# Optimization experiments

Hardware: AMD Instinct MI355X
Metric: run time of the kernel (lower is better)

## Reference

```python
import jax, jax.numpy as jnp
import numpy as np

TEMPERATURE = 0.07
B, D = 8192, 512
NUM_CLASSES = 100


def setup_inputs() -> dict:
    key = jax.random.key(0)
    k1, k2 = jax.random.split(key)
    x = jax.random.normal(k1, (B, D), dtype=jnp.float32)
    # docstring: embeddings are normalized over D
    embeds = x / jnp.linalg.norm(x, axis=-1, keepdims=True)
    labels = jax.random.randint(k2, (B,), 0, NUM_CLASSES, dtype=jnp.int64)
    return {"embeds": embeds, "labels": labels}


def reference(embeds, labels):
    n = embeds.shape[0]
    logits = (embeds @ embeds.T) / TEMPERATURE  # (B, B)
    same_label = labels[None, :] == labels[:, None]  # (B, B), symmetric
    neg_inf = jnp.array(-jnp.inf, dtype=logits.dtype)
    # denominator base: logsumexp over different-label entries of each column
    denom_activations = jnp.where(same_label, neg_inf, logits)
    base_denom_row = jax.nn.logsumexp(denom_activations, axis=0)  # (B,)
    # base_denom[i, j] = base_denom_row[i] (torch code repeats along dim 1)
    in_numer = same_label & ~jnp.eye(n, dtype=bool)
    numer_count = in_numer.sum(axis=0)  # (B,) positives per column
    # log_denom = logaddexp(logit, base) on in_numer entries; ce = log_denom - logit
    log_denom = jnp.logaddexp(logits, base_denom_row[:, None])
    ce = jnp.where(in_numer, log_denom - logits, 0.0)
    loss = jnp.sum(ce / numer_count.astype(ce.dtype)) / n
    return loss
```

## Files before the change

### kernel.cpp

```cpp
#include <hip/hip_runtime.h>
#include <hip/hip_bf16.h>
#include <math.h>

#define NB 8192
#define ND 512
#define NCLS 100

constexpr float INV_T = 1.0f / 0.07f;
constexpr float MAXL  = 1.0f / 0.07f;

typedef __attribute__((ext_vector_type(8))) short short8v;
typedef __attribute__((ext_vector_type(4))) float f32x4;

__device__ __forceinline__ ushort f2bf(float x) {
    uint32_t u = __float_as_uint(x);
    uint32_t r = (u + 0x7FFFu + ((u >> 16) & 1u)) >> 16;
    return (ushort)r;
}
__device__ __forceinline__ float bf2f(short v) {
    return __uint_as_float(((uint32_t)(ushort)v) << 16);
}

__global__ __launch_bounds__(256) void setup_kernel(const int* __restrict__ labels,
                                                    int* cls_cnt, int* cls_off,
                                                    int* cls_cur, int* members,
                                                    int* pair_off, double* accum) {
    __shared__ int s_cnt[NCLS];
    const int t = threadIdx.x;
    if (t < NCLS) s_cnt[t] = 0;
    if (t == 0) *accum = 0.0;
    __syncthreads();
    for (int j = t; j < NB; j += blockDim.x) atomicAdd(&s_cnt[labels[j]], 1);
    __syncthreads();
    if (t < NCLS) cls_cnt[t] = s_cnt[t];
    __syncthreads();
    if (t == 0) {
        int off = 0, poff = 0;
        for (int c = 0; c < NCLS; ++c) {
            cls_off[c] = off; cls_cur[c] = off; off += s_cnt[c];
            pair_off[c] = poff; poff += s_cnt[c] * s_cnt[c];
        }
        pair_off[NCLS] = poff;
    }
    __syncthreads();
    for (int j = t; j < NB; j += blockDim.x) {
        const int c = labels[j];
        const int pos = atomicAdd(&cls_cur[c], 1);
        members[pos] = j;
    }
}

__global__ __launch_bounds__(256) void convert_kernel(const float* __restrict__ E,
                                                      ushort* __restrict__ Ebf,
                                                      float* __restrict__ rowsum) {
    const int idx = blockIdx.x * 256 + threadIdx.x;
    const float4 v = ((const float4*)E)[idx];
    ushort4 o;
    o.x = f2bf(v.x); o.y = f2bf(v.y); o.z = f2bf(v.z); o.w = f2bf(v.w);
    ((ushort4*)Ebf)[idx] = o;
    if (idx < NB) rowsum[idx] = 0.f;
}

__global__ __launch_bounds__(256) void pass1_mfma_kernel(const ushort* __restrict__ Ebf,
                                                         const int* __restrict__ labels,
                                                         float* __restrict__ rowsum) {
    __shared__ ushort Atile[128 * 64];
    __shared__ ushort Btile[128 * 64];
    __shared__ float  s_rowsum[128];
    __shared__ int    s_labi[128];
    __shared__ int    s_labj[128];

    const int t    = threadIdx.x;
    const int lane = t & 63;
    const int w    = t >> 6;
    const int wr   = (w >> 1) * 64;
    const int wc   = (w & 1) * 64;
    const int cl   = lane & 15;
    const int rg   = lane >> 4;

    const int j0 = blockIdx.x * 128;
    const int i0 = blockIdx.y * 128;

    if (t < 128) { s_rowsum[t] = 0.f; s_labi[t] = labels[i0 + t]; }
    else         { s_labj[t - 128] = labels[j0 + t - 128]; }

    f32x4 acc[4][4];
    #pragma unroll
    for (int m = 0; m < 4; ++m)
        #pragma unroll
        for (int n = 0; n < 4; ++n)
            acc[m][n] = (f32x4){0.f, 0.f, 0.f, 0.f};

    for (int ks = 0; ks < ND / 64; ++ks) {
        if (ks) __syncthreads();
        {
            const ushort* asrc = Ebf + (size_t)i0 * ND + ks * 64;
            const ushort* bsrc = Ebf + (size_t)j0 * ND + ks * 64;
            #pragma unroll
            for (int q = 0; q < 4; ++q) {
                const int o    = (w * 4 + q) * 1024 + lane * 16;
                const int row  = o >> 7;
                const int slot = (o & 127) >> 4;
                const int sl2  = slot ^ (row & 7);
                __builtin_amdgcn_global_load_lds(
                    (const __attribute__((address_space(1))) unsigned int*)(asrc + row * ND + sl2 * 8),
                    (__attribute__((address_space(3))) unsigned int*)((char*)Atile + (w * 4 + q) * 1024),
                    16, 0, 0);
                __builtin_amdgcn_global_load_lds(
                    (const __attribute__((address_space(1))) unsigned int*)(bsrc + row * ND + sl2 * 8),
                    (__attribute__((address_space(3))) unsigned int*)((char*)Btile + (w * 4 + q) * 1024),
                    16, 0, 0);
            }
        }
        __syncthreads();

        #pragma unroll
        for (int kk = 0; kk < 2; ++kk) {
            short8v a[4], b[4];
            #pragma unroll
            for (int m = 0; m < 4; ++m) {
                const int row = wr + m * 16 + cl;
                const int sl  = (kk * 4 + rg) ^ (row & 7);
                a[m] = *(const short8v*)(Atile + row * 64 + sl * 8);
            }
            #pragma unroll
            for (int n = 0; n < 4; ++n) {
                const int row = wc + n * 16 + cl;
                const int sl  = (kk * 4 + rg) ^ (row & 7);
                b[n] = *(const short8v*)(Btile + row * 64 + sl * 8);
            }
            #pragma unroll
            for (int m = 0; m < 4; ++m)
                #pragma unroll
                for (int n = 0; n < 4; ++n)
                    acc[m][n] = __builtin_amdgcn_mfma_f32_16x16x32_bf16(a[m], b[n], acc[m][n], 0, 0, 0);
        }
    }

    int ljn[4];
    #pragma unroll
    for (int n = 0; n < 4; ++n) ljn[n] = s_labj[wc + n * 16 + cl];

    #pragma unroll
    for (int m = 0; m < 4; ++m) {
        #pragma unroll
        for (int reg = 0; reg < 4; ++reg) {
            const int rloc = wr + m * 16 + rg * 4 + reg;
            const int li   = s_labi[rloc];
            float s = 0.f;
            #pragma unroll
            for (int n = 0; n < 4; ++n) {
                const float d = acc[m][n][reg];
                const float e = __expf(fmaf(d, INV_T, -MAXL));
                s += (ljn[n] != li) ? e : 0.f;
            }
            s += __shfl_xor(s, 1, 64);
            s += __shfl_xor(s, 2, 64);
            s += __shfl_xor(s, 4, 64);
            s += __shfl_xor(s, 8, 64);
            if (cl == 0) atomicAdd(&s_rowsum[rloc], s);
        }
    }
    __syncthreads();
    if (t < 128) atomicAdd(&rowsum[i0 + t], s_rowsum[t]);
}

__global__ __launch_bounds__(256) void pass2_pairs_kernel(const ushort* __restrict__ Ebf,
                                                          const float* __restrict__ rowsum,
                                                          const int* __restrict__ cls_cnt,
                                                          const int* __restrict__ cls_off,
                                                          const int* __restrict__ members,
                                                          const int* __restrict__ pair_off,
                                                          double* __restrict__ accum) {
    __shared__ int    s_off[NCLS + 1];
    __shared__ double sd[4];
    const int t = threadIdx.x;
    for (int k = t; k <= NCLS; k += 256) s_off[k] = pair_off[k];
    __syncthreads();
    const int P = s_off[NCLS];

    const int g  = t >> 3;
    const int s  = t & 7;

    double dlocal = 0.0;
    for (int p = blockIdx.x * 32 + g; p < P; p += gridDim.x * 32) {
        int lo = 0, hi = NCLS - 1;
        while (lo < hi) {
            const int mid = (lo + hi + 1) >> 1;
            if (s_off[mid] <= p) lo = mid; else hi = mid - 1;
        }
        const int c  = lo;
        const int mc = cls_cnt[c];
        const int q  = p - s_off[c];
        const int a  = q / mc;
        const int b  = q - a * mc;
        if (a == b) continue;
        const int i = members[cls_off[c] + a];
        const int j = members[cls_off[c] + b];

        const ushort* ei = Ebf + (size_t)i * ND + s * 8;
        const ushort* ej = Ebf + (size_t)j * ND + s * 8;
        float d = 0.f;
        #pragma unroll
        for (int it = 0; it < 8; ++it) {
            const short8v x = *(const short8v*)(ei + it * 64);
            const short8v y = *(const short8v*)(ej + it * 64);
            #pragma unroll
            for (int e = 0; e < 8; ++e)
                d = fmaf(bf2f(x[e]), bf2f(y[e]), d);
        }
        d += __shfl_xor(d, 1, 64);
        d += __shfl_xor(d, 2, 64);
        d += __shfl_xor(d, 4, 64);
        if (s == 0) {
            const float base = MAXL + logf(rowsum[i]);
            const float xv   = base - d * INV_T;
            const float sp   = fmaxf(xv, 0.f) + log1pf(__expf(-fabsf(xv)));
            dlocal += (double)(sp / (float)(mc - 1));
        }
    }

    #pragma unroll
    for (int o2 = 32; o2 >= 1; o2 >>= 1) dlocal += __shfl_xor(dlocal, o2, 64);
    const int lane = t & 63, w = t >> 6;
    if (lane == 0) sd[w] = dlocal;
    __syncthreads();
    if (t == 0) {
        const double tot = sd[0] + sd[1] + sd[2] + sd[3];
        if (tot != 0.0) atomicAdd(accum, tot);
    }
}

__global__ void finalize_kernel(const double* __restrict__ accum, float* __restrict__ out) {
    if (threadIdx.x == 0 && blockIdx.x == 0)
        out[0] = (float)(accum[0] / (double)NB);
}

#define TI 16
#define TJ 4
#define THREADS 256

__global__ __launch_bounds__(THREADS) void pass1_f32_kernel(const float* __restrict__ E,
                                                            const int* __restrict__ labels,
                                                            float* __restrict__ base_row) {
    __shared__ float e_tile[TI][ND];
    __shared__ int   s_rowlab[TI];
    __shared__ float s_part[4][TI];

    const int t  = threadIdx.x;
    const int i0 = blockIdx.x * TI;

    {
        const float4* src = (const float4*)(E + (size_t)i0 * ND);
        float4* dst = (float4*)(&e_tile[0][0]);
        #pragma unroll
        for (int k = 0; k < (TI * ND / 4) / THREADS; ++k)
            dst[t + k * THREADS] = src[t + k * THREADS];
    }
    if (t < TI) s_rowlab[t] = labels[i0 + t];
    __syncthreads();

    int rowlab[TI];
    #pragma unroll
    for (int r = 0; r < TI; ++r) rowlab[r] = s_rowlab[r];
    float acc[TI];
    #pragma unroll
    for (int r = 0; r < TI; ++r) acc[r] = 0.f;

    for (int jt = 0; jt < NB; jt += THREADS * TJ) {
        float dot[TI][TJ];
        #pragma unroll
        for (int r = 0; r < TI; ++r)
            #pragma unroll
            for (int q = 0; q < TJ; ++q) dot[r][q] = 0.f;
        const float* jp[TJ];
        #pragma unroll
        for (int q = 0; q < TJ; ++q) jp[q] = E + (size_t)(jt + t + q * THREADS) * ND;
        for (int d = 0; d < ND; d += 4) {
            float4 ev[TJ];
            #pragma unroll
            for (int q = 0; q < TJ; ++q) ev[q] = *(const float4*)(jp[q] + d);
            #pragma unroll
            for (int r = 0; r < TI; ++r) {
                const float4 er = *(const float4*)(&e_tile[r][d]);
                #pragma unroll
                for (int q = 0; q < TJ; ++q) {
                    dot[r][q] = fmaf(er.x, ev[q].x, dot[r][q]);
                    dot[r][q] = fmaf(er.y, ev[q].y, dot[r][q]);
                    dot[r][q] = fmaf(er.z, ev[q].z, dot[r][q]);
                    dot[r][q] = fmaf(er.w, ev[q].w, dot[r][q]);
                }
            }
        }
        #pragma unroll
        for (int q = 0; q < TJ; ++q) {
            const int lj = labels[jt + t + q * THREADS];
            #pragma unroll
            for (int r = 0; r < TI; ++r) {
                const float e = __expf(dot[r][q] * INV_T - MAXL);
                acc[r] += (lj != rowlab[r]) ? e : 0.f;
            }
        }
    }
    const int lane = t & 63, wid = t >> 6;
    #pragma unroll
    for (int r = 0; r < TI; ++r) {
        float v = acc[r];
        #pragma unroll
        for (int off = 32; off >= 1; off >>= 1) v += __shfl_down(v, off, 64);
        if (lane == 0) s_part[wid][r] = v;
    }
    __syncthreads();
    if (t < TI) {
        const float tot = s_part[0][t] + s_part[1][t] + s_part[2][t] + s_part[3][t];
        base_row[i0 + t] = MAXL + logf(tot);
    }
}

__global__ __launch_bounds__(256) void pass2_f32_kernel(const float* __restrict__ E,
                                                        const float* __restrict__ base_row,
                                                        const int* __restrict__ cls_cnt,
                                                        const int* __restrict__ cls_off,
                                                        const int* __restrict__ members,
                                                        double* __restrict__ accum) {
    const int c  = blockIdx.x;
    const int mc = cls_cnt[c];
    double local = 0.0;
    if (mc >= 2) {
        const int off = cls_off[c];
        const float inv_cnt = 1.0f / (float)(mc - 1);
        const int npairs = mc * mc;
        for (int p = threadIdx.x; p < npairs; p += blockDim.x) {
            const int a = p / mc, b = p - a * mc;
            if (a == b) continue;
            const int i = members[off + a];
            const int j = members[off + b];
            const float* ei = E + (size_t)i * ND;
            const float* ej = E + (size_t)j * ND;
            float dot = 0.f;
            for (int d = 0; d < ND; d += 4) {
                const float4 x = *(const float4*)(ei + d);
                const float4 y = *(const float4*)(ej + d);
                dot = fmaf(x.x, y.x, dot); dot = fmaf(x.y, y.y, dot);
                dot = fmaf(x.z, y.z, dot); dot = fmaf(x.w, y.w, dot);
            }
            const float xv = base_row[i] - dot * INV_T;
            const float sp = fmaxf(xv, 0.f) + log1pf(__expf(-fabsf(xv)));
            local += (double)(sp * inv_cnt);
        }
    }
    __shared__ double s_d[4];
    const int lane = threadIdx.x & 63, wid = threadIdx.x >> 6;
    #pragma unroll
    for (int off2 = 32; off2 >= 1; off2 >>= 1) local += __shfl_down(local, off2, 64);
    if (lane == 0) s_d[wid] = local;
    __syncthreads();
    if (threadIdx.x == 0) atomicAdd(accum, s_d[0] + s_d[1] + s_d[2] + s_d[3]);
}

extern "C" void kernel_launch(void* const* d_in, const int* in_sizes, int n_in,
                              void* d_out, int out_size, void* d_ws, size_t ws_size,
                              hipStream_t stream) {
    const float* E      = (const float*)d_in[0];
    const int*   labels = (const int*)d_in[1];
    float* out = (float*)d_out;

    char* ws = (char*)d_ws;
    double* accum    = (double*)ws;
    float*  rowsum   = (float*)(ws + 16);
    int*    cls_cnt  = (int*)(ws + 16 + NB * 4);
    int*    cls_off  = cls_cnt + 128;
    int*    cls_cur  = cls_off + 128;
    int*    members  = cls_cur + 128;
    int*    pair_off = members + NB;
    size_t  ebf_off  = ((16 + (size_t)NB * 4 + 512 * 3 + (size_t)NB * 4 + 512) + 63) & ~(size_t)63;
    ushort* Ebf      = (ushort*)(ws + ebf_off);
    const size_t needed = ebf_off + (size_t)NB * ND * 2;

    hipLaunchKernelGGL(setup_kernel, dim3(1), dim3(256), 0, stream,
                       labels, cls_cnt, cls_off, cls_cur, members, pair_off, accum);

    if (ws_size >= needed) {
        hipLaunchKernelGGL(convert_kernel, dim3(NB * ND / 4 / 256), dim3(256), 0, stream,
                           E, Ebf, rowsum);
        hipLaunchKernelGGL(pass1_mfma_kernel, dim3(NB / 128, NB / 128), dim3(256), 0, stream,
                           Ebf, labels, rowsum);
        hipLaunchKernelGGL(pass2_pairs_kernel, dim3(4096), dim3(256), 0, stream,
                           Ebf, rowsum, cls_cnt, cls_off, members, pair_off, accum);
    } else {
        hipLaunchKernelGGL(pass1_f32_kernel, dim3(NB / TI), dim3(THREADS), 0, stream,
                           E, labels, rowsum);
        hipLaunchKernelGGL(pass2_f32_kernel, dim3(NCLS), dim3(256), 0, stream,
                           E, rowsum, cls_cnt, cls_off, members, accum);
    }
    hipLaunchKernelGGL(finalize_kernel, dim3(1), dim3(64), 0, stream, accum, out);
}
```

Before: 296.7 us.

## Exploit Gram matrix symmetry in pass1 to compute only upper-triangle tiles

The pass1 kernel now returns early for tiles below the diagonal and has each remaining off-diagonal tile add both row sums and column sums into rowsum. This uses the symmetry of E·E^T and the label mask to cut the MFMA and exp work roughly in half. The cost is extra column-reduction shuffles, shared atomics and global atomics per tile. Half of the launched blocks also exit immediately, which can leave CUs unevenly loaded.

```diff
diff --git a/kernel.cpp b/kernel.cpp
--- a/kernel.cpp
+++ b/kernel.cpp
@@ -64,9 +64,13 @@
 __global__ __launch_bounds__(256) void pass1_mfma_kernel(const ushort* __restrict__ Ebf,
                                                          const int* __restrict__ labels,
                                                          float* __restrict__ rowsum) {
+    const int bj = blockIdx.x, bi = blockIdx.y;
+    if (bj < bi) return;
+
     __shared__ ushort Atile[128 * 64];
     __shared__ ushort Btile[128 * 64];
     __shared__ float  s_rowsum[128];
+    __shared__ float  s_colsum[128];
     __shared__ int    s_labi[128];
     __shared__ int    s_labj[128];
 
@@ -78,10 +82,10 @@
     const int cl   = lane & 15;
     const int rg   = lane >> 4;
 
-    const int j0 = blockIdx.x * 128;
-    const int i0 = blockIdx.y * 128;
-
-    if (t < 128) { s_rowsum[t] = 0.f; s_labi[t] = labels[i0 + t]; }
+    const int j0 = bj * 128;
+    const int i0 = bi * 128;
+
+    if (t < 128) { s_rowsum[t] = 0.f; s_colsum[t] = 0.f; s_labi[t] = labels[i0 + t]; }
     else         { s_labj[t - 128] = labels[j0 + t - 128]; }
 
     f32x4 acc[4][4];
@@ -141,28 +145,41 @@
     #pragma unroll
     for (int n = 0; n < 4; ++n) ljn[n] = s_labj[wc + n * 16 + cl];
 
+    float cs[4] = {0.f, 0.f, 0.f, 0.f};
     #pragma unroll
     for (int m = 0; m < 4; ++m) {
         #pragma unroll
         for (int reg = 0; reg < 4; ++reg) {
             const int rloc = wr + m * 16 + rg * 4 + reg;
             const int li   = s_labi[rloc];
-            float s = 0.f;
+            float rs = 0.f;
             #pragma unroll
             for (int n = 0; n < 4; ++n) {
                 const float d = acc[m][n][reg];
                 const float e = __expf(fmaf(d, INV_T, -MAXL));
-                s += (ljn[n] != li) ? e : 0.f;
-            }
-            s += __shfl_xor(s, 1, 64);
-            s += __shfl_xor(s, 2, 64);
-            s += __shfl_xor(s, 4, 64);
-            s += __shfl_xor(s, 8, 64);
-            if (cl == 0) atomicAdd(&s_rowsum[rloc], s);
-        }
-    }
-    __syncthreads();
-    if (t < 128) atomicAdd(&rowsum[i0 + t], s_rowsum[t]);
+                const float msk = (ljn[n] != li) ? e : 0.f;
+                rs += msk;
+                cs[n] += msk;
+            }
+            rs += __shfl_xor(rs, 1, 64);
+            rs += __shfl_xor(rs, 2, 64);
+            rs += __shfl_xor(rs, 4, 64);
+            rs += __shfl_xor(rs, 8, 64);
+            if (cl == 0) atomicAdd(&s_rowsum[rloc], rs);
+        }
+    }
+    #pragma unroll
+    for (int n = 0; n < 4; ++n) {
+        float c = cs[n];
+        c += __shfl_xor(c, 16, 64);
+        c += __shfl_xor(c, 32, 64);
+        if (rg == 0) atomicAdd(&s_colsum[wc + n * 16 + cl], c);
+    }
+    __syncthreads();
+    if (t < 128) {
+        atomicAdd(&rowsum[i0 + t], s_rowsum[t]);
+        if (i0 != j0) atomicAdd(&rowsum[j0 + t], s_colsum[t]);
+    }
 }
 
 __global__ __launch_bounds__(256) void pass2_pairs_kernel(const ushort* __restrict__ Ebf,
```

New measurement: 275.4 us. 1.08x faster.
